# Performance work log

Hardware: AMD Instinct MI355X
Metric: run time of the kernel (lower is better)

Reference implementation:

```python
import jax, jax.numpy as jnp
import numpy as np

HIDDEN = 1024
NUM_HEADS = 16
HEAD_DIM = HIDDEN // NUM_HEADS


def setup_inputs() -> dict:
    key = jax.random.key(0)
    ks = jax.random.split(key, 5)
    scale = 1.0 / np.sqrt(HIDDEN)
    x = jax.random.normal(ks[0], (2, 2048, HIDDEN), dtype=jnp.float32)
    qkv_w = jax.random.uniform(ks[1], (3 * HIDDEN, HIDDEN), jnp.float32, -scale, scale)
    qkv_b = jax.random.uniform(ks[2], (3 * HIDDEN,), jnp.float32, -scale, scale)
    out_w = jax.random.uniform(ks[3], (HIDDEN, HIDDEN), jnp.float32, -scale, scale)
    out_b = jax.random.uniform(ks[4], (HIDDEN,), jnp.float32, -scale, scale)
    return {"x": x, "qkv_w": qkv_w, "qkv_b": qkv_b, "out_w": out_w, "out_b": out_b}


def reference(x, qkv_w, qkv_b, out_w, out_b):
    B, S, _ = x.shape
    qkv = jnp.einsum('bsd,ed->bse', x, qkv_w) + qkv_b  # [B,S,3H]
    q, k, v = jnp.split(qkv, 3, axis=-1)
    # [B,S,H] -> [B,nh,S,hd]
    def to_heads(t):
        return t.reshape(B, S, NUM_HEADS, HEAD_DIM).transpose(0, 2, 1, 3)
    q, k, v = to_heads(q), to_heads(k), to_heads(v)
    scores = jnp.einsum('bhqd,bhkd->bhqk', q, k) / np.sqrt(HEAD_DIM).astype(np.float32)
    attn = jax.nn.softmax(scores, axis=-1)
    o = jnp.einsum('bhqk,bhkd->bhqd', attn, v)
    o = o.transpose(0, 2, 1, 3).reshape(B, S, HIDDEN)
    return jnp.einsum('bsd,ed->bse', o, out_w) + out_b
```

## Files before the change

kernel.cpp:

```cpp
#include <hip/hip_runtime.h>
#include <stdint.h>

typedef __bf16 bf16x8 __attribute__((ext_vector_type(8)));
typedef float  f32x4  __attribute__((ext_vector_type(4)));
typedef float  f32x16 __attribute__((ext_vector_type(16)));
typedef unsigned short u16;
typedef unsigned int   u32;

#define B_  2
#define S_  2048
#define H_  1024
#define NH_ 16
#define HD_ 64
#define QSCL 0.18033688011112042f

__device__ __forceinline__ u16 f2bf(float f) {
  u32 u = __builtin_bit_cast(u32, f);
  return (u16)((u + 0x7FFFu + ((u >> 16) & 1u)) >> 16);
}
__device__ __forceinline__ float ex2(float x) { return __builtin_amdgcn_exp2f(x); }
__device__ __forceinline__ u32 cvtpk(float lo, float hi) {
  u32 r; asm("v_cvt_pk_bf16_f32 %0, %1, %2" : "=v"(r) : "v"(lo), "v"(hi)); return r;
}
__device__ __forceinline__ void gload_lds16(const u16* g, u16* lds) {
  __builtin_amdgcn_global_load_lds(
      (__attribute__((address_space(1))) void*)(void*)g,
      (__attribute__((address_space(3))) void*)lds, 16, 0, 0);
}

__global__ void cvt_all(const float* __restrict__ a, const float* __restrict__ b,
                        const float* __restrict__ c, u16* __restrict__ oa,
                        u16* __restrict__ ob, u16* __restrict__ oc) {
  int i = blockIdx.x * 256 + threadIdx.x;
  const float4* src; ushort4* dst; int j;
  if (i < 1048576)      { src = (const float4*)a; dst = (ushort4*)oa; j = i; }
  else if (i < 1835008) { src = (const float4*)b; dst = (ushort4*)ob; j = i - 1048576; }
  else                  { src = (const float4*)c; dst = (ushort4*)oc; j = i - 1835008; }
  const float4 v = src[j];
  ushort4 o;
  o.x = f2bf(v.x); o.y = f2bf(v.y); o.z = f2bf(v.z); o.w = f2bf(v.w);
  dst[j] = o;
}

__global__ __launch_bounds__(256, 2)
void gemm_qkv(const u16* __restrict__ A, const u16* __restrict__ W,
              const float* __restrict__ bias,
              u16* __restrict__ qb, u16* __restrict__ kb, u16* __restrict__ vtb,
              int M, int N, int K)
{
  __shared__ __align__(16) u16 As[128 * 32];
  __shared__ __align__(16) u16 Bs[128 * 32];
  const int tid = threadIdx.x;
  const int w = tid >> 6, l = tid & 63;
  const int lg = l >> 4, lr = l & 15;
  const int wr = w >> 1, wc = w & 1;
  const int tM = blockIdx.y * 128, tN = blockIdx.x * 128;

  f32x4 acc[4][4];
  const f32x4 z4 = {0.f, 0.f, 0.f, 0.f};
#pragma unroll
  for (int m = 0; m < 4; ++m)
#pragma unroll
    for (int n = 0; n < 4; ++n) acc[m][n] = z4;

  for (int k0 = 0; k0 < K; k0 += 32) {
    __syncthreads();
#pragma unroll
    for (int i = 0; i < 2; ++i) {
      const int ch = i * 256 + tid;
      const int row = ch >> 2, cc = (ch & 3) * 8;
      gload_lds16(A + (size_t)(tM + row) * K + k0 + cc, As + (size_t)(i * 256 + w * 64) * 8);
      gload_lds16(W + (size_t)(tN + row) * K + k0 + cc, Bs + (size_t)(i * 256 + w * 64) * 8);
    }
    __syncthreads();
    bf16x8 af[4], bw[4];
#pragma unroll
    for (int m = 0; m < 4; ++m)
      af[m] = *(const bf16x8*)&As[(wr * 64 + m * 16 + lr) * 32 + lg * 8];
#pragma unroll
    for (int n = 0; n < 4; ++n)
      bw[n] = *(const bf16x8*)&Bs[(wc * 64 + n * 16 + lr) * 32 + lg * 8];
#pragma unroll
    for (int m = 0; m < 4; ++m)
#pragma unroll
      for (int n = 0; n < 4; ++n)
        acc[m][n] = __builtin_amdgcn_mfma_f32_16x16x32_bf16(af[m], bw[n], acc[m][n], 0, 0, 0);
  }

#pragma unroll
  for (int n = 0; n < 4; ++n) {
    const int col = tN + wc * 64 + n * 16 + lr;
    const float bv = bias[col];
    const int t3 = col >> 10, rem = col & 1023;
    const int hh = rem >> 6, dd = rem & 63;
    const float sc = (t3 == 0) ? QSCL : 1.f;
    u16* dst = (t3 == 0) ? qb : (t3 == 1) ? kb : vtb;
#pragma unroll
    for (int m = 0; m < 4; ++m)
#pragma unroll
      for (int r = 0; r < 4; ++r) {
        const int row = tM + wr * 64 + m * 16 + lg * 4 + r;
        const int bb = row >> 11, ss = row & 2047;
        const u16 val = f2bf((acc[m][n][r] + bv) * sc);
        if (t3 < 2) dst[((size_t)(bb * NH_ + hh) * S_ + ss) * HD_ + dd] = val;
        else        dst[((size_t)(bb * NH_ + hh) * HD_ + dd) * S_ + ss] = val;
      }
  }
}

__global__ __launch_bounds__(256, 2)
void gemm_out(const u16* __restrict__ A, const u16* __restrict__ W,
              const float* __restrict__ bias, float* __restrict__ outf,
              int M, int N, int K)
{
  __shared__ __align__(16) u16 As[128 * 32];
  __shared__ __align__(16) u16 Bs[64 * 32];
  const int tid = threadIdx.x;
  const int w = tid >> 6, l = tid & 63;
  const int lg = l >> 4, lr = l & 15;
  const int tM = blockIdx.y * 128, tN = blockIdx.x * 64;

  f32x4 acc[2][4];
  const f32x4 z4 = {0.f, 0.f, 0.f, 0.f};
#pragma unroll
  for (int m = 0; m < 2; ++m)
#pragma unroll
    for (int n = 0; n < 4; ++n) acc[m][n] = z4;

  for (int k0 = 0; k0 < K; k0 += 32) {
    __syncthreads();
#pragma unroll
    for (int i = 0; i < 2; ++i) {
      const int ch = i * 256 + tid;
      const int row = ch >> 2, cc = (ch & 3) * 8;
      gload_lds16(A + (size_t)(tM + row) * K + k0 + cc, As + (size_t)(i * 256 + w * 64) * 8);
    }
    gload_lds16(W + (size_t)(tN + (tid >> 2)) * K + k0 + (tid & 3) * 8, Bs + (size_t)(w * 64) * 8);
    __syncthreads();
    bf16x8 af[2], bw[4];
#pragma unroll
    for (int m = 0; m < 2; ++m)
      af[m] = *(const bf16x8*)&As[(w * 32 + m * 16 + lr) * 32 + lg * 8];
#pragma unroll
    for (int n = 0; n < 4; ++n)
      bw[n] = *(const bf16x8*)&Bs[(n * 16 + lr) * 32 + lg * 8];
#pragma unroll
    for (int m = 0; m < 2; ++m)
#pragma unroll
      for (int n = 0; n < 4; ++n)
        acc[m][n] = __builtin_amdgcn_mfma_f32_16x16x32_bf16(af[m], bw[n], acc[m][n], 0, 0, 0);
  }

#pragma unroll
  for (int n = 0; n < 4; ++n) {
    const int col = tN + n * 16 + lr;
    const float bv = bias[col];
#pragma unroll
    for (int m = 0; m < 2; ++m)
#pragma unroll
      for (int r = 0; r < 4; ++r) {
        const int row = tM + w * 32 + m * 16 + lg * 4 + r;
        outf[(size_t)row * N + col] = acc[m][n][r] + bv;
      }
  }
}

__global__ __launch_bounds__(256, 2)
void attn_fwd(const u16* __restrict__ qb, const u16* __restrict__ kb,
              const u16* __restrict__ vtb, u16* __restrict__ ob)
{
  __shared__ __align__(16) u16 Kl[2][64 * 64];
  __shared__ __align__(16) u16 Vl[2][64 * 64];

  const int tid = threadIdx.x;
  const int w = tid >> 6, l = tid & 63;
  const int q32 = l & 31, hi = l >> 5;
  const int idx = blockIdx.x;
  const int bh = idx & 31, qt = idx >> 5;
  const int bb = bh >> 4, hh = bh & 15;
  const int q0 = qt * 128 + w * 32;

  bf16x8 qf[4];
#pragma unroll
  for (int ks = 0; ks < 4; ++ks)
    qf[ks] = *(const bf16x8*)&qb[((size_t)bh * S_ + q0 + q32) * HD_ + ks * 16 + hi * 8];

  const f32x16 z16 = {};
  f32x16 acc[2] = {z16, z16};
  float lrun = 0.f;

  const int srow = l >> 3;
  const int scol = ((l & 7) ^ srow) << 3;
  const u16* kbase = kb  + ((size_t)bh * S_  + w * 16 + srow) * HD_ + scol;
  const u16* vbase = vtb + ((size_t)bh * HD_ + w * 16 + srow) * S_  + scol;

  auto STAGE = [&](int buf, int t) {
#pragma unroll
    for (int j = 0; j < 2; ++j) {
      gload_lds16(kbase + (size_t)t * 64 * HD_ + j * 8 * HD_, &Kl[buf][(w * 16 + j * 8) * 64]);
      gload_lds16(vbase + (size_t)t * 64 + j * 8 * S_,        &Vl[buf][(w * 16 + j * 8) * 64]);
    }
  };

  STAGE(0, 0);
  __syncthreads();

  const int sw = q32 & 7;

  for (int t = 0; t < 32; ++t) {
    const int cur = t & 1;
    if (t + 1 < 32) STAGE(cur ^ 1, t + 1);

    f32x16 st[2] = {z16, z16};
    __builtin_amdgcn_s_setprio(1);
#pragma unroll
    for (int kt = 0; kt < 2; ++kt)
#pragma unroll
      for (int ks = 0; ks < 4; ++ks) {
        const bf16x8 kf = *(const bf16x8*)&Kl[cur][(kt * 32 + q32) * 64 + ((((ks << 1) | hi) ^ sw) << 3)];
        st[kt] = __builtin_amdgcn_mfma_f32_32x32x16_bf16(kf, qf[ks], st[kt], 0, 0, 0);
      }
    __builtin_amdgcn_s_setprio(0);

    bf16x8 pa[4];
#pragma unroll
    for (int kt = 0; kt < 2; ++kt) {
      float p[16];
#pragma unroll
      for (int r = 0; r < 16; ++r) p[r] = ex2(st[kt][r]);
#pragma unroll
      for (int g = 0; g < 4; ++g)
        lrun += (p[4 * g] + p[4 * g + 1]) + (p[4 * g + 2] + p[4 * g + 3]);
      u32 wk0[4], wk1[4];
#pragma unroll
      for (int g = 0; g < 4; ++g) {
        wk0[g] = cvtpk(p[4 * g], p[4 * g + 1]);
        wk1[g] = cvtpk(p[4 * g + 2], p[4 * g + 3]);
      }
#pragma unroll
      for (int k2 = 0; k2 < 2; ++k2) {
        u32 a0 = wk0[2 * k2], b0 = wk0[2 * k2 + 1];
        u32 a1 = wk1[2 * k2], b1 = wk1[2 * k2 + 1];
        asm volatile("v_permlane32_swap_b32 %0, %1" : "+v"(a0), "+v"(b0));
        asm volatile("v_permlane32_swap_b32 %0, %1" : "+v"(a1), "+v"(b1));
        uint4 wv = {a0, a1, b0, b1};
        pa[kt * 2 + k2] = __builtin_bit_cast(bf16x8, wv);
      }
    }

    __builtin_amdgcn_s_setprio(1);
#pragma unroll
    for (int dt = 0; dt < 2; ++dt)
#pragma unroll
      for (int ks = 0; ks < 4; ++ks) {
        const bf16x8 vf = *(const bf16x8*)&Vl[cur][(dt * 32 + q32) * 64 + ((((ks << 1) | hi) ^ sw) << 3)];
        acc[dt] = __builtin_amdgcn_mfma_f32_32x32x16_bf16(vf, pa[ks], acc[dt], 0, 0, 0);
      }
    __builtin_amdgcn_s_setprio(0);

    __syncthreads();
  }

  lrun += __shfl_xor(lrun, 32);
  const float linv = 1.f / lrun;
  const size_t orow = ((size_t)(bb * S_ + q0 + q32)) * H_ + hh * HD_;
#pragma unroll
  for (int dt = 0; dt < 2; ++dt)
#pragma unroll
    for (int g = 0; g < 4; ++g) {
      const u32 o0 = cvtpk(acc[dt][4 * g] * linv, acc[dt][4 * g + 1] * linv);
      const u32 o1 = cvtpk(acc[dt][4 * g + 2] * linv, acc[dt][4 * g + 3] * linv);
      uint2 ov; ov.x = o0; ov.y = o1;
      *(uint2*)&ob[orow + dt * 32 + g * 8 + hi * 4] = ov;
    }
}

extern "C" void kernel_launch(void* const* d_in, const int* in_sizes, int n_in,
                              void* d_out, int out_size, void* d_ws, size_t ws_size,
                              hipStream_t stream) {
  const float* x     = (const float*)d_in[0];
  const float* qkv_w = (const float*)d_in[1];
  const float* qkv_b = (const float*)d_in[2];
  const float* out_w = (const float*)d_in[3];
  const float* out_b = (const float*)d_in[4];

  char* ws = (char*)d_ws;
  u16* xb    = (u16*)(ws);
  u16* wqkvb = (u16*)(ws + 8388608);
  u16* wob   = (u16*)(ws + 14680064);
  u16* qb    = (u16*)(ws + 16777216);
  u16* kb    = (u16*)(ws + 25165824);
  u16* vtb   = (u16*)(ws + 33554432);
  u16* ob    = (u16*)(ws + 41943040);

  cvt_all<<<8192, 256, 0, stream>>>(x, qkv_w, out_w, xb, wqkvb, wob);

  gemm_qkv<<<dim3(24, 32), 256, 0, stream>>>(xb, wqkvb, qkv_b,
                                             qb, kb, vtb, 4096, 3072, 1024);
  attn_fwd<<<512, 256, 0, stream>>>(qb, kb, vtb, ob);
  gemm_out<<<dim3(16, 32), 256, 0, stream>>>(ob, wob, out_b, (float*)d_out,
                                             4096, 1024, 1024);
}
```

Baseline: 117.7 us.

## Double-buffer GEMM LDS staging and move V transpose to separate kernel

Both GEMMs now use two LDS buffers and prefetch the next K-slice while computing on the current one, which removes one barrier per iteration and overlaps global loads with MFMA work. The QKV epilogue writes V in the same row-major head layout as Q and K, avoiding strided transposed stores. A new vtrans kernel then transposes V through LDS into the x-bf16 buffer, which is reused since it is no longer needed. This adds an extra launch and an extra V read/write pass, and doubles LDS use per block.

```diff
diff --git a/kernel.cpp b/kernel.cpp
--- a/kernel.cpp
+++ b/kernel.cpp
@@ -45,11 +45,11 @@
 __global__ __launch_bounds__(256, 2)
 void gemm_qkv(const u16* __restrict__ A, const u16* __restrict__ W,
               const float* __restrict__ bias,
-              u16* __restrict__ qb, u16* __restrict__ kb, u16* __restrict__ vtb,
+              u16* __restrict__ qb, u16* __restrict__ kb, u16* __restrict__ vb,
               int M, int N, int K)
 {
-  __shared__ __align__(16) u16 As[128 * 32];
-  __shared__ __align__(16) u16 Bs[128 * 32];
+  __shared__ __align__(16) u16 As[2][128 * 32];
+  __shared__ __align__(16) u16 Bs[2][128 * 32];
   const int tid = threadIdx.x;
   const int w = tid >> 6, l = tid & 63;
   const int lg = l >> 4, lr = l & 15;
@@ -63,28 +63,35 @@
 #pragma unroll
     for (int n = 0; n < 4; ++n) acc[m][n] = z4;
 
-  for (int k0 = 0; k0 < K; k0 += 32) {
-    __syncthreads();
+  auto STG = [&](int buf, int k0) {
 #pragma unroll
     for (int i = 0; i < 2; ++i) {
       const int ch = i * 256 + tid;
       const int row = ch >> 2, cc = (ch & 3) * 8;
-      gload_lds16(A + (size_t)(tM + row) * K + k0 + cc, As + (size_t)(i * 256 + w * 64) * 8);
-      gload_lds16(W + (size_t)(tN + row) * K + k0 + cc, Bs + (size_t)(i * 256 + w * 64) * 8);
-    }
-    __syncthreads();
+      gload_lds16(A + (size_t)(tM + row) * K + k0 + cc, As[buf] + (size_t)(i * 256 + w * 64) * 8);
+      gload_lds16(W + (size_t)(tN + row) * K + k0 + cc, Bs[buf] + (size_t)(i * 256 + w * 64) * 8);
+    }
+  };
+
+  STG(0, 0);
+  __syncthreads();
+
+  for (int it = 0; it < K / 32; ++it) {
+    const int cur = it & 1;
+    if (it + 1 < K / 32) STG(cur ^ 1, (it + 1) * 32);
     bf16x8 af[4], bw[4];
 #pragma unroll
     for (int m = 0; m < 4; ++m)
-      af[m] = *(const bf16x8*)&As[(wr * 64 + m * 16 + lr) * 32 + lg * 8];
+      af[m] = *(const bf16x8*)&As[cur][(wr * 64 + m * 16 + lr) * 32 + lg * 8];
 #pragma unroll
     for (int n = 0; n < 4; ++n)
-      bw[n] = *(const bf16x8*)&Bs[(wc * 64 + n * 16 + lr) * 32 + lg * 8];
+      bw[n] = *(const bf16x8*)&Bs[cur][(wc * 64 + n * 16 + lr) * 32 + lg * 8];
 #pragma unroll
     for (int m = 0; m < 4; ++m)
 #pragma unroll
       for (int n = 0; n < 4; ++n)
         acc[m][n] = __builtin_amdgcn_mfma_f32_16x16x32_bf16(af[m], bw[n], acc[m][n], 0, 0, 0);
+    __syncthreads();
   }
 
 #pragma unroll
@@ -94,17 +101,39 @@
     const int t3 = col >> 10, rem = col & 1023;
     const int hh = rem >> 6, dd = rem & 63;
     const float sc = (t3 == 0) ? QSCL : 1.f;
-    u16* dst = (t3 == 0) ? qb : (t3 == 1) ? kb : vtb;
+    u16* dst = (t3 == 0) ? qb : (t3 == 1) ? kb : vb;
 #pragma unroll
     for (int m = 0; m < 4; ++m)
 #pragma unroll
       for (int r = 0; r < 4; ++r) {
         const int row = tM + wr * 64 + m * 16 + lg * 4 + r;
         const int bb = row >> 11, ss = row & 2047;
-        const u16 val = f2bf((acc[m][n][r] + bv) * sc);
-        if (t3 < 2) dst[((size_t)(bb * NH_ + hh) * S_ + ss) * HD_ + dd] = val;
-        else        dst[((size_t)(bb * NH_ + hh) * HD_ + dd) * S_ + ss] = val;
-      }
+        dst[((size_t)(bb * NH_ + hh) * S_ + ss) * HD_ + dd] = f2bf((acc[m][n][r] + bv) * sc);
+      }
+  }
+}
+
+__global__ __launch_bounds__(256, 4)
+void vtrans(const u16* __restrict__ vb, u16* __restrict__ vtb)
+{
+  __shared__ u16 Ls[64 * 65];
+  const int t = threadIdx.x;
+  const int bh = blockIdx.y;
+  const int s0 = blockIdx.x * 64;
+  const u16* src = vb + ((size_t)bh * S_ + s0) * HD_;
+  const int d = t & 63, sy = t >> 6;
+#pragma unroll
+  for (int p = 0; p < 16; ++p) {
+    const int s = p * 4 + sy;
+    Ls[s * 65 + d] = src[(size_t)s * HD_ + d];
+  }
+  __syncthreads();
+  const int s = t & 63, dy = t >> 6;
+  u16* dst = vtb + (size_t)bh * HD_ * S_ + s0;
+#pragma unroll
+  for (int p = 0; p < 16; ++p) {
+    const int dd = p * 4 + dy;
+    dst[(size_t)dd * S_ + s] = Ls[s * 65 + dd];
   }
 }
 
@@ -113,8 +142,8 @@
               const float* __restrict__ bias, float* __restrict__ outf,
               int M, int N, int K)
 {
-  __shared__ __align__(16) u16 As[128 * 32];
-  __shared__ __align__(16) u16 Bs[64 * 32];
+  __shared__ __align__(16) u16 As[2][128 * 32];
+  __shared__ __align__(16) u16 Bs[2][64 * 32];
   const int tid = threadIdx.x;
   const int w = tid >> 6, l = tid & 63;
   const int lg = l >> 4, lr = l & 15;
@@ -127,28 +156,35 @@
 #pragma unroll
     for (int n = 0; n < 4; ++n) acc[m][n] = z4;
 
-  for (int k0 = 0; k0 < K; k0 += 32) {
-    __syncthreads();
+  auto STG = [&](int buf, int k0) {
 #pragma unroll
     for (int i = 0; i < 2; ++i) {
       const int ch = i * 256 + tid;
       const int row = ch >> 2, cc = (ch & 3) * 8;
-      gload_lds16(A + (size_t)(tM + row) * K + k0 + cc, As + (size_t)(i * 256 + w * 64) * 8);
-    }
-    gload_lds16(W + (size_t)(tN + (tid >> 2)) * K + k0 + (tid & 3) * 8, Bs + (size_t)(w * 64) * 8);
-    __syncthreads();
+      gload_lds16(A + (size_t)(tM + row) * K + k0 + cc, As[buf] + (size_t)(i * 256 + w * 64) * 8);
+    }
+    gload_lds16(W + (size_t)(tN + (tid >> 2)) * K + k0 + (tid & 3) * 8, Bs[buf] + (size_t)(w * 64) * 8);
+  };
+
+  STG(0, 0);
+  __syncthreads();
+
+  for (int it = 0; it < K / 32; ++it) {
+    const int cur = it & 1;
+    if (it + 1 < K / 32) STG(cur ^ 1, (it + 1) * 32);
     bf16x8 af[2], bw[4];
 #pragma unroll
     for (int m = 0; m < 2; ++m)
-      af[m] = *(const bf16x8*)&As[(w * 32 + m * 16 + lr) * 32 + lg * 8];
+      af[m] = *(const bf16x8*)&As[cur][(w * 32 + m * 16 + lr) * 32 + lg * 8];
 #pragma unroll
     for (int n = 0; n < 4; ++n)
-      bw[n] = *(const bf16x8*)&Bs[(n * 16 + lr) * 32 + lg * 8];
+      bw[n] = *(const bf16x8*)&Bs[cur][(n * 16 + lr) * 32 + lg * 8];
 #pragma unroll
     for (int m = 0; m < 2; ++m)
 #pragma unroll
       for (int n = 0; n < 4; ++n)
         acc[m][n] = __builtin_amdgcn_mfma_f32_16x16x32_bf16(af[m], bw[n], acc[m][n], 0, 0, 0);
+    __syncthreads();
   }
 
 #pragma unroll
@@ -290,13 +326,15 @@
   u16* wob   = (u16*)(ws + 14680064);
   u16* qb    = (u16*)(ws + 16777216);
   u16* kb    = (u16*)(ws + 25165824);
-  u16* vtb   = (u16*)(ws + 33554432);
+  u16* vb    = (u16*)(ws + 33554432);
   u16* ob    = (u16*)(ws + 41943040);
+  u16* vtb   = xb;
 
   cvt_all<<<8192, 256, 0, stream>>>(x, qkv_w, out_w, xb, wqkvb, wob);
 
   gemm_qkv<<<dim3(24, 32), 256, 0, stream>>>(xb, wqkvb, qkv_b,
-                                             qb, kb, vtb, 4096, 3072, 1024);
+                                             qb, kb, vb, 4096, 3072, 1024);
+  vtrans<<<dim3(32, 32), 256, 0, stream>>>(vb, vtb);
   attn_fwd<<<512, 256, 0, stream>>>(qb, kb, vtb, ob);
   gemm_out<<<dim3(16, 32), 256, 0, stream>>>(ob, wob, out_b, (float*)d_out,
                                              4096, 1024, 1024);
```

New measurement: 117.9 us. About the same (+0.2%).
